# Optimization experiments

Hardware: AMD Instinct MI355X
Metric: run time of the kernel (lower is better)

## Reference

```python
import jax, jax.numpy as jnp
import numpy as np

NUM_EMB = 1024
EMB_DIM = 64


def setup_inputs() -> dict:
    key = jax.random.key(0)
    k1, k2 = jax.random.split(key)
    x = jax.random.normal(k1, (32, EMB_DIM, 4096), dtype=jnp.float32)
    # nn.Embedding weight initialized uniform(-1/K, 1/K)
    emb = jax.random.uniform(k2, (NUM_EMB, EMB_DIM), dtype=jnp.float32,
                             minval=-1.0 / NUM_EMB, maxval=1.0 / NUM_EMB)
    return {"x": x, "emb": emb}


def reference(x, emb):
    D = emb.shape[1]
    # Faithful to torch .view(-1, D): raw row-major flatten of contiguous x
    xf = x.reshape(-1, D)                                   # [N, D]
    # ||xf||^2 + ||e||^2 - 2 xf e^T  (cdist^2 via matmul)
    d = (jnp.sum(xf * xf, axis=1, keepdims=True)
         + jnp.sum(emb * emb, axis=1)
         - 2.0 * xf @ emb.T)                                # [N, K]
    idx = jnp.argmin(d, axis=1)                             # [N] int
    idx = idx.reshape((x.shape[0],) + x.shape[2:])          # [B, T]
    quantized = emb[idx].reshape(x.shape)                   # raw reshape, as view_as
    return quantized, idx
```

## Files before the change

### kernel.cpp

```cpp
#include <hip/hip_runtime.h>


#define N_ROWS   131072
#define NUM_EMB  1024
#define EMB_DIM  64
#define Q_ELEMS  8388608
#define THREADS  512
#define ROWS_PB  256
#define KCHUNK   128
#define NCHUNKS  8
#define WCAP     2048

typedef short short8 __attribute__((ext_vector_type(8)));
typedef float f32x4  __attribute__((ext_vector_type(4)));

__device__ __forceinline__ unsigned short bf16_rne(float f) {
    unsigned u = __float_as_uint(f);
    u += 0x7fffu + ((u >> 16) & 1u);
    return (unsigned short)(u >> 16);
}

__device__ __forceinline__ unsigned fkey(float d) {
    unsigned b = __float_as_uint(d);
    return b ^ (((unsigned)((int)b >> 31)) | 0x80000000u);
}

__device__ __forceinline__ float np_sq64(const float* a) {
    #pragma clang fp contract(off)
    float r0=a[0]*a[0],r1=a[1]*a[1],r2=a[2]*a[2],r3=a[3]*a[3];
    float r4=a[4]*a[4],r5=a[5]*a[5],r6=a[6]*a[6],r7=a[7]*a[7];
    #pragma unroll
    for (int i=8;i<64;i+=8){
        r0+=a[i+0]*a[i+0];r1+=a[i+1]*a[i+1];r2+=a[i+2]*a[i+2];r3+=a[i+3]*a[i+3];
        r4+=a[i+4]*a[i+4];r5+=a[i+5]*a[i+5];r6+=a[i+6]*a[i+6];r7+=a[i+7]*a[i+7];
    }
    return ((r0+r1)+(r2+r3))+((r4+r5)+(r6+r7));
}

__device__ __forceinline__ float rotmin16(float v) {
    int x;
    x = __builtin_amdgcn_update_dpp(0, __float_as_int(v), 0x121, 0xf, 0xf, true);
    v = fminf(v, __int_as_float(x));
    x = __builtin_amdgcn_update_dpp(0, __float_as_int(v), 0x122, 0xf, 0xf, true);
    v = fminf(v, __int_as_float(x));
    x = __builtin_amdgcn_update_dpp(0, __float_as_int(v), 0x124, 0xf, 0xf, true);
    v = fminf(v, __int_as_float(x));
    x = __builtin_amdgcn_update_dpp(0, __float_as_int(v), 0x128, 0xf, 0xf, true);
    v = fminf(v, __int_as_float(x));
    return v;
}

__global__ __launch_bounds__(256) void vq_prep(const float* __restrict__ emb,
                                               float* __restrict__ sume,
                                               unsigned short* __restrict__ ehg) {
    int k = blockIdx.x * 256 + threadIdx.x;
    if (k < NUM_EMB) {
        sume[k] = np_sq64(emb + (k << 6));
        int c = k >> 7, krow = k & 127;
        #pragma unroll
        for (int gp = 0; gp < 8; ++gp) {
            short8 h;
            #pragma unroll
            for (int j = 0; j < 8; ++j)
                h[j] = (short)bf16_rne(emb[(k << 6) + gp*8 + j]);
            reinterpret_cast<short8*>(ehg)[c*1024 + gp*128 + krow] = h;
        }
    }
}

__global__ __launch_bounds__(THREADS, 4)
void vq_main(const float* __restrict__ x, const float* __restrict__ emb,
             const float* __restrict__ sume_g, const unsigned short* __restrict__ ehg,
             float* __restrict__ out_q, float* __restrict__ out_idx) {
    __shared__ int4     EH4[1024];
    __shared__ float    SUME[NUM_EMB];
    __shared__ float    RMIN[ROWS_PB];
    __shared__ float    THR[ROWS_PB];
    __shared__ float    SA[ROWS_PB];
    __shared__ int      WL[WCAP];
    __shared__ float    WLD[WCAP];
    __shared__ unsigned DMIN[ROWS_PB];
    __shared__ unsigned KMIN[ROWS_PB];
    __shared__ int      SIDX[ROWS_PB];
    __shared__ unsigned WCNT;

    const int t   = threadIdx.x;
    const int w   = t >> 6;
    const int l   = t & 63;
    const int g   = l >> 4;
    const int c16 = l & 15;
    const size_t blk_row0 = (size_t)blockIdx.x * ROWS_PB;

    SUME[t]       = sume_g[t];
    SUME[t + 512] = sume_g[t + 512];

    short8 ah[2][2];
    #pragma unroll
    for (int s = 0; s < 2; ++s) {
        const float* xp = x + (blk_row0 + (size_t)(w*32 + s*16 + c16)) * EMB_DIM;
        float sabs = 0.f;
        #pragma unroll
        for (int hf = 0; hf < 2; ++hf) {
            #pragma unroll
            for (int j = 0; j < 8; ++j) {
                float v = 2.0f * xp[hf*32 + g*8 + j];
                sabs += fabsf(v);
                ah[s][hf][j] = (short)bf16_rne(v);
            }
        }
        sabs += __shfl_xor(sabs, 16);
        sabs += __shfl_xor(sabs, 32);
        if (g == 0) SA[w*32 + s*16 + c16] = sabs;
    }

    float stash[2][4];
    #pragma unroll
    for (int s = 0; s < 2; ++s) {
        #pragma unroll
        for (int r = 0; r < 4; ++r) stash[s][r] = 3.4e38f;
    }

    for (int c = 0; c < NCHUNKS; ++c) {
        __syncthreads();
        EH4[t]       = reinterpret_cast<const int4*>(ehg)[c*1024 + t];
        EH4[t + 512] = reinterpret_cast<const int4*>(ehg)[c*1024 + t + 512];
        __syncthreads();
        #pragma unroll
        for (int lt = 0; lt < 8; ++lt) {
            const int krow = lt*16 + c16;
            short8 bh0 = reinterpret_cast<const short8*>(EH4)[(g    )*128 + krow];
            short8 bh1 = reinterpret_cast<const short8*>(EH4)[(g + 4)*128 + krow];
            float scol = SUME[c*KCHUNK + krow];
            f32x4 a0 = {0.f,0.f,0.f,0.f}, a1 = {0.f,0.f,0.f,0.f};
            a0 = __builtin_amdgcn_mfma_f32_16x16x32_bf16(ah[0][0], bh0, a0, 0,0,0);
            a1 = __builtin_amdgcn_mfma_f32_16x16x32_bf16(ah[1][0], bh0, a1, 0,0,0);
            a0 = __builtin_amdgcn_mfma_f32_16x16x32_bf16(ah[0][1], bh1, a0, 0,0,0);
            a1 = __builtin_amdgcn_mfma_f32_16x16x32_bf16(ah[1][1], bh1, a1, 0,0,0);
            #pragma unroll
            for (int r = 0; r < 4; ++r) {
                stash[0][r] = fminf(stash[0][r], scol - a0[r]);
                stash[1][r] = fminf(stash[1][r], scol - a1[r]);
            }
        }
    }
    #pragma unroll
    for (int s = 0; s < 2; ++s) {
        #pragma unroll
        for (int r = 0; r < 4; ++r) {
            float v = rotmin16(stash[s][r]);
            if (c16 == 0) RMIN[w*32 + s*16 + 4*g + r] = v;
        }
    }
    __syncthreads();
    if (t < ROWS_PB) {
        THR[t]  = RMIN[t] + (SA[t] * 1.6e-5f + 4.0e-5f);
        DMIN[t] = 0xFFFFFFFFu;
        KMIN[t] = 0xFFFFFFFFu;
    }
    if (t == 0) WCNT = 0u;
    __syncthreads();

    float thrv[2][4];
    #pragma unroll
    for (int s = 0; s < 2; ++s) {
        #pragma unroll
        for (int r = 0; r < 4; ++r)
            thrv[s][r] = THR[w*32 + s*16 + 4*g + r];
    }

    for (int c = 0; c < NCHUNKS; ++c) {
        __syncthreads();
        EH4[t]       = reinterpret_cast<const int4*>(ehg)[c*1024 + t];
        EH4[t + 512] = reinterpret_cast<const int4*>(ehg)[c*1024 + t + 512];
        __syncthreads();
        #pragma unroll
        for (int lt = 0; lt < 8; ++lt) {
            const int krow = lt*16 + c16;
            short8 bh0 = reinterpret_cast<const short8*>(EH4)[(g    )*128 + krow];
            short8 bh1 = reinterpret_cast<const short8*>(EH4)[(g + 4)*128 + krow];
            float scol = SUME[c*KCHUNK + krow];
            f32x4 a0 = {0.f,0.f,0.f,0.f}, a1 = {0.f,0.f,0.f,0.f};
            a0 = __builtin_amdgcn_mfma_f32_16x16x32_bf16(ah[0][0], bh0, a0, 0,0,0);
            a1 = __builtin_amdgcn_mfma_f32_16x16x32_bf16(ah[1][0], bh0, a1, 0,0,0);
            a0 = __builtin_amdgcn_mfma_f32_16x16x32_bf16(ah[0][1], bh1, a0, 0,0,0);
            a1 = __builtin_amdgcn_mfma_f32_16x16x32_bf16(ah[1][1], bh1, a1, 0,0,0);
            const int kk = c*KCHUNK + krow;
            #pragma unroll
            for (int r = 0; r < 4; ++r) {
                float sv0 = scol - a0[r];
                if (sv0 < thrv[0][r]) {
                    unsigned p = atomicAdd(&WCNT, 1u);
                    if (p < WCAP) WL[p] = ((w*32 + 4*g + r) << 10) | kk;
                }
                float sv1 = scol - a1[r];
                if (sv1 < thrv[1][r]) {
                    unsigned p = atomicAdd(&WCNT, 1u);
                    if (p < WCAP) WL[p] = ((w*32 + 16 + 4*g + r) << 10) | kk;
                }
            }
        }
    }
    __syncthreads();
    const unsigned wc = WCNT;

    if (wc <= WCAP) {
        for (unsigned p = t; p < wc; p += THREADS) {
            int pr = WL[p]; int row = pr >> 10; int kk = pr & 1023;
            const float* xr = x + (blk_row0 + (size_t)row) * EMB_DIM;
            const float* er = emb + (kk << 6);
            float sumx = np_sq64(xr);
            float cc = 0.f;
            #pragma unroll 8
            for (int i = 0; i < EMB_DIM; ++i)
                cc = fmaf(2.0f * xr[i], er[i], cc);
            float d;
            {
                #pragma clang fp contract(off)
                d = (sumx + sume_g[kk]) - cc;
            }
            WLD[p] = d;
            atomicMin(&DMIN[row], fkey(d));
        }
        __syncthreads();
        for (unsigned p = t; p < wc; p += THREADS) {
            int pr = WL[p]; int row = pr >> 10; int kk = pr & 1023;
            if (fkey(WLD[p]) == DMIN[row])
                atomicMin(&KMIN[row], (unsigned)kk);
        }
        __syncthreads();
        if (t < ROWS_PB) {
            int bk = (int)KMIN[t];
            SIDX[t] = bk;
            out_idx[blk_row0 + t] = (float)bk;
        }
    } else {
        if (t < ROWS_PB) {
            const float* xr = x + (blk_row0 + (size_t)t) * EMB_DIM;
            float sumx = np_sq64(xr);
            volatile const float* xv = xr;
            float bm = 3.4e38f; int bb = 0;
            for (int kk = 0; kk < NUM_EMB; ++kk) {
                const float* er = emb + (kk << 6);
                float cc = 0.f;
                for (int i = 0; i < EMB_DIM; ++i)
                    cc = fmaf(2.0f * xv[i], er[i], cc);
                {
                    #pragma clang fp contract(off)
                    float d = (sumx + sume_g[kk]) - cc;
                    if (d < bm) { bm = d; bb = kk; }
                }
            }
            SIDX[t] = bb;
            out_idx[blk_row0 + t] = (float)bb;
        }
    }
    __syncthreads();

    const float4* emb4 = reinterpret_cast<const float4*>(emb);
    float4* q4 = reinterpret_cast<float4*>(out_q + blk_row0 * EMB_DIM);
    #pragma unroll
    for (int i = 0; i < 8; ++i) {
        int e4 = t + i * THREADS;
        int rr = e4 >> 4, cc2 = e4 & 15;
        q4[e4] = emb4[SIDX[rr]*16 + cc2];
    }
}

extern "C" void kernel_launch(void* const* d_in, const int* in_sizes, int n_in,
                              void* d_out, int out_size, void* d_ws, size_t ws_size,
                              hipStream_t stream) {
    const float* x   = (const float*)d_in[0];
    const float* emb = (const float*)d_in[1];
    float* out_q   = (float*)d_out;
    float* out_idx = out_q + Q_ELEMS;
    float*          sume = (float*)d_ws;
    unsigned short* ehg  = (unsigned short*)((char*)d_ws + 4096);

    vq_prep<<<dim3(NUM_EMB / 256), dim3(256), 0, stream>>>(emb, sume, ehg);
    vq_main<<<dim3(N_ROWS / ROWS_PB), dim3(THREADS), 0, stream>>>(x, emb, sume, ehg,
                                                                  out_q, out_idx);
}
```

Measured before the change: 82.48 us.

## Fuse two-pass VQ candidate search into single pass with running-min threshold

Replaces the two MFMA passes over the codebook (one to find the approximate min, one to collect candidates) with a single pass. That pass keeps a running row minimum via cross-lane shuffles and emits candidates whose approximate distance falls below the current running threshold. It double-buffers the codebook chunks in LDS with register prefetch, swaps the MFMA operand order so each lane holds four consecutive codes of one row, and reuses the EH4 buffer for candidate distances. Halving the matrix work and the syncs comes at the cost of more candidates, since early running minima are loose. WCAP is raised to match, launch bounds drop to 2 waves per SIMD, and more candidates mean more exact-refinement work and atomics.

Measured after the change: 135.6 us. +64.4%, slower.

```diff
diff --git a/kernel.cpp b/kernel.cpp
--- a/kernel.cpp
+++ b/kernel.cpp
@@ -9,7 +9,7 @@
 #define ROWS_PB  256
 #define KCHUNK   128
 #define NCHUNKS  8
-#define WCAP     2048
+#define WCAP     6144
 
 typedef short short8 __attribute__((ext_vector_type(8)));
 typedef float f32x4  __attribute__((ext_vector_type(4)));
@@ -35,19 +35,6 @@
         r4+=a[i+4]*a[i+4];r5+=a[i+5]*a[i+5];r6+=a[i+6]*a[i+6];r7+=a[i+7]*a[i+7];
     }
     return ((r0+r1)+(r2+r3))+((r4+r5)+(r6+r7));
-}
-
-__device__ __forceinline__ float rotmin16(float v) {
-    int x;
-    x = __builtin_amdgcn_update_dpp(0, __float_as_int(v), 0x121, 0xf, 0xf, true);
-    v = fminf(v, __int_as_float(x));
-    x = __builtin_amdgcn_update_dpp(0, __float_as_int(v), 0x122, 0xf, 0xf, true);
-    v = fminf(v, __int_as_float(x));
-    x = __builtin_amdgcn_update_dpp(0, __float_as_int(v), 0x124, 0xf, 0xf, true);
-    v = fminf(v, __int_as_float(x));
-    x = __builtin_amdgcn_update_dpp(0, __float_as_int(v), 0x128, 0xf, 0xf, true);
-    v = fminf(v, __int_as_float(x));
-    return v;
 }
 
 __global__ __launch_bounds__(256) void vq_prep(const float* __restrict__ emb,
@@ -68,17 +55,13 @@
     }
 }
 
-__global__ __launch_bounds__(THREADS, 4)
+__global__ __launch_bounds__(THREADS, 2)
 void vq_main(const float* __restrict__ x, const float* __restrict__ emb,
              const float* __restrict__ sume_g, const unsigned short* __restrict__ ehg,
              float* __restrict__ out_q, float* __restrict__ out_idx) {
-    __shared__ int4     EH4[1024];
+    __shared__ int4     EH4[2][1024];
     __shared__ float    SUME[NUM_EMB];
-    __shared__ float    RMIN[ROWS_PB];
-    __shared__ float    THR[ROWS_PB];
-    __shared__ float    SA[ROWS_PB];
     __shared__ int      WL[WCAP];
-    __shared__ float    WLD[WCAP];
     __shared__ unsigned DMIN[ROWS_PB];
     __shared__ unsigned KMIN[ROWS_PB];
     __shared__ int      SIDX[ROWS_PB];
@@ -93,8 +76,11 @@
 
     SUME[t]       = sume_g[t];
     SUME[t + 512] = sume_g[t + 512];
+    if (t < ROWS_PB) { DMIN[t] = 0xFFFFFFFFu; KMIN[t] = 0xFFFFFFFFu; }
+    if (t == 0) WCNT = 0u;
 
     short8 ah[2][2];
+    float  thr[2];
     #pragma unroll
     for (int s = 0; s < 2; ++s) {
         const float* xp = x + (blk_row0 + (size_t)(w*32 + s*16 + c16)) * EMB_DIM;
@@ -110,102 +96,69 @@
         }
         sabs += __shfl_xor(sabs, 16);
         sabs += __shfl_xor(sabs, 32);
-        if (g == 0) SA[w*32 + s*16 + c16] = sabs;
-    }
-
-    float stash[2][4];
-    #pragma unroll
-    for (int s = 0; s < 2; ++s) {
-        #pragma unroll
-        for (int r = 0; r < 4; ++r) stash[s][r] = 3.4e38f;
-    }
-
+        thr[s] = sabs * 1.6e-5f + 4.0e-5f;
+    }
+
+    float rm0 = 3.4e38f, rm1 = 3.4e38f;
+
+    const int4* eg4 = reinterpret_cast<const int4*>(ehg);
+    int4 sa = eg4[t], sb = eg4[t + 512];
+    EH4[0][t] = sa; EH4[0][t + 512] = sb;
+    if (NCHUNKS > 1) { sa = eg4[1024 + t]; sb = eg4[1024 + t + 512]; }
+    __syncthreads();
+
+    int p = 0;
     for (int c = 0; c < NCHUNKS; ++c) {
-        __syncthreads();
-        EH4[t]       = reinterpret_cast<const int4*>(ehg)[c*1024 + t];
-        EH4[t + 512] = reinterpret_cast<const int4*>(ehg)[c*1024 + t + 512];
-        __syncthreads();
+        if (c + 1 < NCHUNKS) {
+            EH4[p^1][t] = sa; EH4[p^1][t + 512] = sb;
+            if (c + 2 < NCHUNKS) {
+                sa = eg4[(c+2)*1024 + t]; sb = eg4[(c+2)*1024 + t + 512];
+            }
+        }
         #pragma unroll
         for (int lt = 0; lt < 8; ++lt) {
             const int krow = lt*16 + c16;
-            short8 bh0 = reinterpret_cast<const short8*>(EH4)[(g    )*128 + krow];
-            short8 bh1 = reinterpret_cast<const short8*>(EH4)[(g + 4)*128 + krow];
-            float scol = SUME[c*KCHUNK + krow];
+            short8 ea0 = *reinterpret_cast<const short8*>(&EH4[p][(g    )*128 + krow]);
+            short8 ea1 = *reinterpret_cast<const short8*>(&EH4[p][(g + 4)*128 + krow]);
+            const int kb = c*KCHUNK + lt*16 + 4*g;
+            f32x4 sm4 = *reinterpret_cast<const f32x4*>(&SUME[kb]);
             f32x4 a0 = {0.f,0.f,0.f,0.f}, a1 = {0.f,0.f,0.f,0.f};
-            a0 = __builtin_amdgcn_mfma_f32_16x16x32_bf16(ah[0][0], bh0, a0, 0,0,0);
-            a1 = __builtin_amdgcn_mfma_f32_16x16x32_bf16(ah[1][0], bh0, a1, 0,0,0);
-            a0 = __builtin_amdgcn_mfma_f32_16x16x32_bf16(ah[0][1], bh1, a0, 0,0,0);
-            a1 = __builtin_amdgcn_mfma_f32_16x16x32_bf16(ah[1][1], bh1, a1, 0,0,0);
-            #pragma unroll
-            for (int r = 0; r < 4; ++r) {
-                stash[0][r] = fminf(stash[0][r], scol - a0[r]);
-                stash[1][r] = fminf(stash[1][r], scol - a1[r]);
-            }
-        }
-    }
-    #pragma unroll
-    for (int s = 0; s < 2; ++s) {
-        #pragma unroll
-        for (int r = 0; r < 4; ++r) {
-            float v = rotmin16(stash[s][r]);
-            if (c16 == 0) RMIN[w*32 + s*16 + 4*g + r] = v;
-        }
-    }
-    __syncthreads();
-    if (t < ROWS_PB) {
-        THR[t]  = RMIN[t] + (SA[t] * 1.6e-5f + 4.0e-5f);
-        DMIN[t] = 0xFFFFFFFFu;
-        KMIN[t] = 0xFFFFFFFFu;
-    }
-    if (t == 0) WCNT = 0u;
-    __syncthreads();
-
-    float thrv[2][4];
-    #pragma unroll
-    for (int s = 0; s < 2; ++s) {
-        #pragma unroll
-        for (int r = 0; r < 4; ++r)
-            thrv[s][r] = THR[w*32 + s*16 + 4*g + r];
-    }
-
-    for (int c = 0; c < NCHUNKS; ++c) {
+            a0 = __builtin_amdgcn_mfma_f32_16x16x32_bf16(ea0, ah[0][0], a0, 0,0,0);
+            a1 = __builtin_amdgcn_mfma_f32_16x16x32_bf16(ea0, ah[1][0], a1, 0,0,0);
+            a0 = __builtin_amdgcn_mfma_f32_16x16x32_bf16(ea1, ah[0][1], a0, 0,0,0);
+            a1 = __builtin_amdgcn_mfma_f32_16x16x32_bf16(ea1, ah[1][1], a1, 0,0,0);
+            float s00 = sm4[0]-a0[0], s01 = sm4[1]-a0[1],
+                  s02 = sm4[2]-a0[2], s03 = sm4[3]-a0[3];
+            float s10 = sm4[0]-a1[0], s11 = sm4[1]-a1[1],
+                  s12 = sm4[2]-a1[2], s13 = sm4[3]-a1[3];
+            rm0 = fminf(rm0, fminf(fminf(s00,s01), fminf(s02,s03)));
+            rm1 = fminf(rm1, fminf(fminf(s10,s11), fminf(s12,s13)));
+            rm0 = fminf(rm0, __shfl_xor(rm0, 16));
+            rm0 = fminf(rm0, __shfl_xor(rm0, 32));
+            rm1 = fminf(rm1, __shfl_xor(rm1, 16));
+            rm1 = fminf(rm1, __shfl_xor(rm1, 32));
+            const float t0 = rm0 + thr[0], t1 = rm1 + thr[1];
+            const int row0 = (w*32 +      c16) << 10;
+            const int row1 = (w*32 + 16 + c16) << 10;
+            if (s00 < t0) { unsigned q = atomicAdd(&WCNT,1u); if (q < WCAP) WL[q] = row0 | (kb+0); }
+            if (s01 < t0) { unsigned q = atomicAdd(&WCNT,1u); if (q < WCAP) WL[q] = row0 | (kb+1); }
+            if (s02 < t0) { unsigned q = atomicAdd(&WCNT,1u); if (q < WCAP) WL[q] = row0 | (kb+2); }
+            if (s03 < t0) { unsigned q = atomicAdd(&WCNT,1u); if (q < WCAP) WL[q] = row0 | (kb+3); }
+            if (s10 < t1) { unsigned q = atomicAdd(&WCNT,1u); if (q < WCAP) WL[q] = row1 | (kb+0); }
+            if (s11 < t1) { unsigned q = atomicAdd(&WCNT,1u); if (q < WCAP) WL[q] = row1 | (kb+1); }
+            if (s12 < t1) { unsigned q = atomicAdd(&WCNT,1u); if (q < WCAP) WL[q] = row1 | (kb+2); }
+            if (s13 < t1) { unsigned q = atomicAdd(&WCNT,1u); if (q < WCAP) WL[q] = row1 | (kb+3); }
+        }
         __syncthreads();
-        EH4[t]       = reinterpret_cast<const int4*>(ehg)[c*1024 + t];
-        EH4[t + 512] = reinterpret_cast<const int4*>(ehg)[c*1024 + t + 512];
-        __syncthreads();
-        #pragma unroll
-        for (int lt = 0; lt < 8; ++lt) {
-            const int krow = lt*16 + c16;
-            short8 bh0 = reinterpret_cast<const short8*>(EH4)[(g    )*128 + krow];
-            short8 bh1 = reinterpret_cast<const short8*>(EH4)[(g + 4)*128 + krow];
-            float scol = SUME[c*KCHUNK + krow];
-            f32x4 a0 = {0.f,0.f,0.f,0.f}, a1 = {0.f,0.f,0.f,0.f};
-            a0 = __builtin_amdgcn_mfma_f32_16x16x32_bf16(ah[0][0], bh0, a0, 0,0,0);
-            a1 = __builtin_amdgcn_mfma_f32_16x16x32_bf16(ah[1][0], bh0, a1, 0,0,0);
-            a0 = __builtin_amdgcn_mfma_f32_16x16x32_bf16(ah[0][1], bh1, a0, 0,0,0);
-            a1 = __builtin_amdgcn_mfma_f32_16x16x32_bf16(ah[1][1], bh1, a1, 0,0,0);
-            const int kk = c*KCHUNK + krow;
-            #pragma unroll
-            for (int r = 0; r < 4; ++r) {
-                float sv0 = scol - a0[r];
-                if (sv0 < thrv[0][r]) {
-                    unsigned p = atomicAdd(&WCNT, 1u);
-                    if (p < WCAP) WL[p] = ((w*32 + 4*g + r) << 10) | kk;
-                }
-                float sv1 = scol - a1[r];
-                if (sv1 < thrv[1][r]) {
-                    unsigned p = atomicAdd(&WCNT, 1u);
-                    if (p < WCAP) WL[p] = ((w*32 + 16 + 4*g + r) << 10) | kk;
-                }
-            }
-        }
-    }
-    __syncthreads();
+        p ^= 1;
+    }
+
     const unsigned wc = WCNT;
+    float* WLD = reinterpret_cast<float*>(EH4);
 
     if (wc <= WCAP) {
-        for (unsigned p = t; p < wc; p += THREADS) {
-            int pr = WL[p]; int row = pr >> 10; int kk = pr & 1023;
+        for (unsigned q = t; q < wc; q += THREADS) {
+            int pr = WL[q]; int row = pr >> 10; int kk = pr & 1023;
             const float* xr = x + (blk_row0 + (size_t)row) * EMB_DIM;
             const float* er = emb + (kk << 6);
             float sumx = np_sq64(xr);
@@ -216,15 +169,15 @@
             float d;
             {
                 #pragma clang fp contract(off)
-                d = (sumx + sume_g[kk]) - cc;
-            }
-            WLD[p] = d;
+                d = (sumx + SUME[kk]) - cc;
+            }
+            WLD[q] = d;
             atomicMin(&DMIN[row], fkey(d));
         }
         __syncthreads();
-        for (unsigned p = t; p < wc; p += THREADS) {
-            int pr = WL[p]; int row = pr >> 10; int kk = pr & 1023;
-            if (fkey(WLD[p]) == DMIN[row])
+        for (unsigned q = t; q < wc; q += THREADS) {
+            int pr = WL[q]; int row = pr >> 10; int kk = pr & 1023;
+            if (fkey(WLD[q]) == DMIN[row])
                 atomicMin(&KMIN[row], (unsigned)kk);
         }
         __syncthreads();
@@ -246,7 +199,7 @@
                     cc = fmaf(2.0f * xv[i], er[i], cc);
                 {
                     #pragma clang fp contract(off)
-                    float d = (sumx + sume_g[kk]) - cc;
+                    float d = (sumx + SUME[kk]) - cc;
                     if (d < bm) { bm = d; bb = kk; }
                 }
             }
```

## Halve rows per block, prefetch codebook chunks into registers, alias WLD onto LDS

Applied to the files above, without the earlier changes.

Cuts rows per block from 256 to 128, which doubles the grid and raises launch_bounds occupancy from 4 to 8 blocks. Each warp now handles 16 rows with one MFMA pair per tile instead of two. The codebook chunk loads are register-prefetched so the global fetch of chunk c+1 overlaps the MFMA work on chunk c. WLD is aliased onto the EH4 LDS buffer and SUME is read from LDS instead of global memory in the rescoring step, which cuts shared-memory footprint. The trade-off is twice the codebook traffic per row, since each block rereads all chunks twice for half as many rows, and a smaller candidate cap that may fall back more often to the slow exact path.

Result: no change. 83.17 us (+0.8%).

```diff
diff --git a/kernel.cpp b/kernel.cpp
--- a/kernel.cpp
+++ b/kernel.cpp
@@ -6,10 +6,10 @@
 #define EMB_DIM  64
 #define Q_ELEMS  8388608
 #define THREADS  512
-#define ROWS_PB  256
+#define ROWS_PB  128
 #define KCHUNK   128
 #define NCHUNKS  8
-#define WCAP     2048
+#define WCAP     1024
 
 typedef short short8 __attribute__((ext_vector_type(8)));
 typedef float f32x4  __attribute__((ext_vector_type(4)));
@@ -68,7 +68,7 @@
     }
 }
 
-__global__ __launch_bounds__(THREADS, 4)
+__global__ __launch_bounds__(THREADS, 8)
 void vq_main(const float* __restrict__ x, const float* __restrict__ emb,
              const float* __restrict__ sume_g, const unsigned short* __restrict__ ehg,
              float* __restrict__ out_q, float* __restrict__ out_idx) {
@@ -78,7 +78,6 @@
     __shared__ float    THR[ROWS_PB];
     __shared__ float    SA[ROWS_PB];
     __shared__ int      WL[WCAP];
-    __shared__ float    WLD[WCAP];
     __shared__ unsigned DMIN[ROWS_PB];
     __shared__ unsigned KMIN[ROWS_PB];
     __shared__ int      SIDX[ROWS_PB];
@@ -91,13 +90,17 @@
     const int c16 = l & 15;
     const size_t blk_row0 = (size_t)blockIdx.x * ROWS_PB;
 
+    const int4* eg4 = reinterpret_cast<const int4*>(ehg);
+    int4 sa = eg4[t], sb = eg4[t + 512];
+
     SUME[t]       = sume_g[t];
     SUME[t + 512] = sume_g[t + 512];
-
-    short8 ah[2][2];
-    #pragma unroll
-    for (int s = 0; s < 2; ++s) {
-        const float* xp = x + (blk_row0 + (size_t)(w*32 + s*16 + c16)) * EMB_DIM;
+    if (t < ROWS_PB) { DMIN[t] = 0xFFFFFFFFu; KMIN[t] = 0xFFFFFFFFu; }
+    if (t == 0) WCNT = 0u;
+
+    short8 ah[2];
+    {
+        const float* xp = x + (blk_row0 + (size_t)(w*16 + c16)) * EMB_DIM;
         float sabs = 0.f;
         #pragma unroll
         for (int hf = 0; hf < 2; ++hf) {
@@ -105,107 +108,87 @@
             for (int j = 0; j < 8; ++j) {
                 float v = 2.0f * xp[hf*32 + g*8 + j];
                 sabs += fabsf(v);
-                ah[s][hf][j] = (short)bf16_rne(v);
+                ah[hf][j] = (short)bf16_rne(v);
             }
         }
         sabs += __shfl_xor(sabs, 16);
         sabs += __shfl_xor(sabs, 32);
-        if (g == 0) SA[w*32 + s*16 + c16] = sabs;
-    }
-
-    float stash[2][4];
-    #pragma unroll
-    for (int s = 0; s < 2; ++s) {
-        #pragma unroll
-        for (int r = 0; r < 4; ++r) stash[s][r] = 3.4e38f;
-    }
+        if (g == 0) SA[w*16 + c16] = sabs;
+    }
+
+    float stash[4] = {3.4e38f, 3.4e38f, 3.4e38f, 3.4e38f};
 
     for (int c = 0; c < NCHUNKS; ++c) {
-        __syncthreads();
-        EH4[t]       = reinterpret_cast<const int4*>(ehg)[c*1024 + t];
-        EH4[t + 512] = reinterpret_cast<const int4*>(ehg)[c*1024 + t + 512];
-        __syncthreads();
+        EH4[t] = sa; EH4[t + 512] = sb;
+        __syncthreads();
+        if (c + 1 < NCHUNKS) {
+            sa = eg4[(c+1)*1024 + t]; sb = eg4[(c+1)*1024 + t + 512];
+        }
         #pragma unroll
         for (int lt = 0; lt < 8; ++lt) {
             const int krow = lt*16 + c16;
             short8 bh0 = reinterpret_cast<const short8*>(EH4)[(g    )*128 + krow];
             short8 bh1 = reinterpret_cast<const short8*>(EH4)[(g + 4)*128 + krow];
             float scol = SUME[c*KCHUNK + krow];
-            f32x4 a0 = {0.f,0.f,0.f,0.f}, a1 = {0.f,0.f,0.f,0.f};
-            a0 = __builtin_amdgcn_mfma_f32_16x16x32_bf16(ah[0][0], bh0, a0, 0,0,0);
-            a1 = __builtin_amdgcn_mfma_f32_16x16x32_bf16(ah[1][0], bh0, a1, 0,0,0);
-            a0 = __builtin_amdgcn_mfma_f32_16x16x32_bf16(ah[0][1], bh1, a0, 0,0,0);
-            a1 = __builtin_amdgcn_mfma_f32_16x16x32_bf16(ah[1][1], bh1, a1, 0,0,0);
-            #pragma unroll
-            for (int r = 0; r < 4; ++r) {
-                stash[0][r] = fminf(stash[0][r], scol - a0[r]);
-                stash[1][r] = fminf(stash[1][r], scol - a1[r]);
-            }
-        }
-    }
-    #pragma unroll
-    for (int s = 0; s < 2; ++s) {
-        #pragma unroll
-        for (int r = 0; r < 4; ++r) {
-            float v = rotmin16(stash[s][r]);
-            if (c16 == 0) RMIN[w*32 + s*16 + 4*g + r] = v;
-        }
+            f32x4 a0 = {0.f,0.f,0.f,0.f};
+            a0 = __builtin_amdgcn_mfma_f32_16x16x32_bf16(ah[0], bh0, a0, 0,0,0);
+            a0 = __builtin_amdgcn_mfma_f32_16x16x32_bf16(ah[1], bh1, a0, 0,0,0);
+            #pragma unroll
+            for (int r = 0; r < 4; ++r)
+                stash[r] = fminf(stash[r], scol - a0[r]);
+        }
+        __syncthreads();
+    }
+
+    #pragma unroll
+    for (int r = 0; r < 4; ++r) {
+        float v = rotmin16(stash[r]);
+        if (c16 == 0) RMIN[w*16 + 4*g + r] = v;
     }
     __syncthreads();
     if (t < ROWS_PB) {
-        THR[t]  = RMIN[t] + (SA[t] * 1.6e-5f + 4.0e-5f);
-        DMIN[t] = 0xFFFFFFFFu;
-        KMIN[t] = 0xFFFFFFFFu;
-    }
-    if (t == 0) WCNT = 0u;
+        THR[t] = RMIN[t] + (SA[t] * 1.6e-5f + 4.0e-5f);
+    }
     __syncthreads();
-
-    float thrv[2][4];
-    #pragma unroll
-    for (int s = 0; s < 2; ++s) {
-        #pragma unroll
-        for (int r = 0; r < 4; ++r)
-            thrv[s][r] = THR[w*32 + s*16 + 4*g + r];
-    }
-
+    float thrv[4];
+    #pragma unroll
+    for (int r = 0; r < 4; ++r) thrv[r] = THR[w*16 + 4*g + r];
+
+    sa = eg4[t]; sb = eg4[t + 512];
     for (int c = 0; c < NCHUNKS; ++c) {
-        __syncthreads();
-        EH4[t]       = reinterpret_cast<const int4*>(ehg)[c*1024 + t];
-        EH4[t + 512] = reinterpret_cast<const int4*>(ehg)[c*1024 + t + 512];
-        __syncthreads();
+        EH4[t] = sa; EH4[t + 512] = sb;
+        __syncthreads();
+        if (c + 1 < NCHUNKS) {
+            sa = eg4[(c+1)*1024 + t]; sb = eg4[(c+1)*1024 + t + 512];
+        }
         #pragma unroll
         for (int lt = 0; lt < 8; ++lt) {
             const int krow = lt*16 + c16;
             short8 bh0 = reinterpret_cast<const short8*>(EH4)[(g    )*128 + krow];
             short8 bh1 = reinterpret_cast<const short8*>(EH4)[(g + 4)*128 + krow];
             float scol = SUME[c*KCHUNK + krow];
-            f32x4 a0 = {0.f,0.f,0.f,0.f}, a1 = {0.f,0.f,0.f,0.f};
-            a0 = __builtin_amdgcn_mfma_f32_16x16x32_bf16(ah[0][0], bh0, a0, 0,0,0);
-            a1 = __builtin_amdgcn_mfma_f32_16x16x32_bf16(ah[1][0], bh0, a1, 0,0,0);
-            a0 = __builtin_amdgcn_mfma_f32_16x16x32_bf16(ah[0][1], bh1, a0, 0,0,0);
-            a1 = __builtin_amdgcn_mfma_f32_16x16x32_bf16(ah[1][1], bh1, a1, 0,0,0);
+            f32x4 a0 = {0.f,0.f,0.f,0.f};
+            a0 = __builtin_amdgcn_mfma_f32_16x16x32_bf16(ah[0], bh0, a0, 0,0,0);
+            a0 = __builtin_amdgcn_mfma_f32_16x16x32_bf16(ah[1], bh1, a0, 0,0,0);
             const int kk = c*KCHUNK + krow;
             #pragma unroll
             for (int r = 0; r < 4; ++r) {
-                float sv0 = scol - a0[r];
-                if (sv0 < thrv[0][r]) {
-                    unsigned p = atomicAdd(&WCNT, 1u);
-                    if (p < WCAP) WL[p] = ((w*32 + 4*g + r) << 10) | kk;
+                float sv = scol - a0[r];
+                if (sv < thrv[r]) {
+                    unsigned q = atomicAdd(&WCNT, 1u);
+                    if (q < WCAP) WL[q] = ((w*16 + 4*g + r) << 10) | kk;
                 }
-                float sv1 = scol - a1[r];
-                if (sv1 < thrv[1][r]) {
-                    unsigned p = atomicAdd(&WCNT, 1u);
-                    if (p < WCAP) WL[p] = ((w*32 + 16 + 4*g + r) << 10) | kk;
-                }
-            }
-        }
-    }
-    __syncthreads();
+            }
+        }
+        __syncthreads();
+    }
+
     const unsigned wc = WCNT;
+    float* WLD = reinterpret_cast<float*>(EH4);
 
     if (wc <= WCAP) {
-        for (unsigned p = t; p < wc; p += THREADS) {
-            int pr = WL[p]; int row = pr >> 10; int kk = pr & 1023;
+        for (unsigned q = t; q < wc; q += THREADS) {
+            int pr = WL[q]; int row = pr >> 10; int kk = pr & 1023;
             const float* xr = x + (blk_row0 + (size_t)row) * EMB_DIM;
             const float* er = emb + (kk << 6);
             float sumx = np_sq64(xr);
@@ -216,15 +199,15 @@
             float d;
             {
                 #pragma clang fp contract(off)
-                d = (sumx + sume_g[kk]) - cc;
-            }
-            WLD[p] = d;
+                d = (sumx + SUME[kk]) - cc;
+            }
+            WLD[q] = d;
             atomicMin(&DMIN[row], fkey(d));
         }
         __syncthreads();
-        for (unsigned p = t; p < wc; p += THREADS) {
-            int pr = WL[p]; int row = pr >> 10; int kk = pr & 1023;
-            if (fkey(WLD[p]) == DMIN[row])
+        for (unsigned q = t; q < wc; q += THREADS) {
+            int pr = WL[q]; int row = pr >> 10; int kk = pr & 1023;
+            if (fkey(WLD[q]) == DMIN[row])
                 atomicMin(&KMIN[row], (unsigned)kk);
         }
         __syncthreads();
@@ -246,7 +229,7 @@
                     cc = fmaf(2.0f * xv[i], er[i], cc);
                 {
                     #pragma clang fp contract(off)
-                    float d = (sumx + sume_g[kk]) - cc;
+                    float d = (sumx + SUME[kk]) - cc;
                     if (d < bm) { bm = d; bb = kk; }
                 }
             }
@@ -259,7 +242,7 @@
     const float4* emb4 = reinterpret_cast<const float4*>(emb);
     float4* q4 = reinterpret_cast<float4*>(out_q + blk_row0 * EMB_DIM);
     #pragma unroll
-    for (int i = 0; i < 8; ++i) {
+    for (int i = 0; i < 4; ++i) {
         int e4 = t + i * THREADS;
         int rr = e4 >> 4, cc2 = e4 & 15;
         q4[e4] = emb4[SIDX[rr]*16 + cc2];
```
